# Kernel tuning notes

Hardware: AMD Instinct MI355X
Metric: run time of the kernel (lower is better)

## Reference

```python
import jax, jax.numpy as jnp
import numpy as np

D_MODEL = 768
NHEAD = 12
HEAD_DIM = D_MODEL // NHEAD
WINDOW = 33  # band half-width = 16


def setup_inputs() -> dict:
    key = jax.random.key(0)
    ks = jax.random.split(key, 9)
    B, T, C = 2, 4096, D_MODEL
    s = 0.02
    return {
        "x": jax.random.normal(ks[0], (B, T, C), jnp.float32),
        "Wq": jax.random.normal(ks[1], (C, C), jnp.float32) * s,
        "bq": jnp.zeros((C,), jnp.float32),
        "Wk": jax.random.normal(ks[2], (C, C), jnp.float32) * s,
        "bk": jnp.zeros((C,), jnp.float32),
        "Wv": jax.random.normal(ks[3], (C, C), jnp.float32) * s,
        "bv": jnp.zeros((C,), jnp.float32),
        "Wo": jax.random.normal(ks[4], (C, C), jnp.float32) * s,
        "bo": jnp.zeros((C,), jnp.float32),
    }


def reference(x, Wq, bq, Wk, bk, Wv, bv, Wo, bo):
    B, T, C = x.shape
    H, D = NHEAD, HEAD_DIM
    scale = D ** -0.5
    # torch Linear: x @ W.T + b
    q = (x @ Wq.T + bq).reshape(B, T, H, D).transpose(0, 2, 1, 3)  # [B,H,T,D]
    k = (x @ Wk.T + bk).reshape(B, T, H, D).transpose(0, 2, 1, 3)
    v = (x @ Wv.T + bv).reshape(B, T, H, D).transpose(0, 2, 1, 3)
    scores = jnp.einsum("bhqd,bhkd->bhqk", q, k) * scale  # [B,H,T,T]
    idx = jnp.arange(T)
    local_mask = jnp.abs(idx[:, None] - idx[None, :]) <= (WINDOW // 2)  # [T,T]
    scores = jnp.where(local_mask[None, None], scores, -jnp.inf)
    attn = jax.nn.softmax(scores, axis=-1)  # dropout=0 / eval mode
    out = jnp.einsum("bhqk,bhkd->bhqd", attn, v)  # [B,H,T,D]
    out = out.transpose(0, 2, 1, 3).reshape(B, T, C)
    return out @ Wo.T + bo
```

## Files before the change

### kernel.cpp

```cpp
#include <hip/hip_runtime.h>
#include <math.h>
#include <cstdint>
#include <cstddef>

typedef unsigned short u16;
typedef short bf16x8 __attribute__((ext_vector_type(8)));
typedef float f32x4 __attribute__((ext_vector_type(4)));
typedef u16 u16x8 __attribute__((ext_vector_type(8)));
typedef u16 u16x4 __attribute__((ext_vector_type(4)));

#define T_LEN 4096
#define NH 12
#define HD 64
#define DMODEL 768
#define GK 768
#define QKV_STRIDE 6291456ul

__device__ __forceinline__ u16 f2bf(float x) {
  union { float f; unsigned u; } v; v.f = x;
  unsigned r = v.u + 0x7fffu + ((v.u >> 16) & 1u);
  return (u16)(r >> 16);
}

__device__ __forceinline__ void async16(const u16* g, u16* l) {
  __builtin_amdgcn_global_load_lds(
      (const __attribute__((address_space(1))) unsigned int*)g,
      (__attribute__((address_space(3))) unsigned int*)l, 16, 0, 0);
}

__global__ void cvt_all(const float* __restrict__ x,
                        const float* __restrict__ Wq, const float* __restrict__ Wk,
                        const float* __restrict__ Wv, const float* __restrict__ Wo,
                        u16* __restrict__ xb, u16* __restrict__ wqkv, u16* __restrict__ wo_b) {
  int bx = blockIdx.x;
  const float* s; u16* d; int base;
  if (bx < 6144)      { s = x;  d = xb;             base = bx; }
  else if (bx < 6720) { s = Wq; d = wqkv;           base = bx - 6144; }
  else if (bx < 7296) { s = Wk; d = wqkv + 589824;  base = bx - 6720; }
  else if (bx < 7872) { s = Wv; d = wqkv + 1179648; base = bx - 7296; }
  else                { s = Wo; d = wo_b;           base = bx - 7872; }
  int i = (base * 256 + (int)threadIdx.x) * 4;
  float4 v = *(const float4*)(s + i);
  u16x4 o;
  o[0] = f2bf(v.x); o[1] = f2bf(v.y); o[2] = f2bf(v.z); o[3] = f2bf(v.w);
  *(u16x4*)(d + i) = o;
}

#define BN 128
#define BK 32
#define CPAD 8

template <int EPI, int MI, int NX, int NW>
__global__ __launch_bounds__(NW * 64)
void gemm_bt(const u16* __restrict__ A, const u16* __restrict__ B,
             const float* __restrict__ bias0, const float* __restrict__ bias1,
             const float* __restrict__ bias2, void* __restrict__ outp) {
  constexpr int NT   = NW * 64;
  constexpr int BMt  = (NW == 8) ? 256 : MI * 32;
  constexpr int NSTEP = GK / BK;
  constexpr int PER = NX / 8;
  constexpr int STG = 3 * (BMt + BN) * BK * 2;
  constexpr int CSZ = (EPI == 3) ? BMt * (BN + CPAD) * 2
                                 : 64 * 132 * 4;
  constexpr int SMEM = STG > CSZ ? STG : CSZ;
  __shared__ __align__(16) char smem[SMEM];
  u16* AsB = (u16*)smem;
  u16* BsB = (u16*)smem + 3 * BMt * BK;

  const int bid  = blockIdx.x;
  const int xcd  = bid & 7;
  const int slot = bid >> 3;
  const int bx   = xcd * PER + (slot % PER);
  const int by   = slot / PER;

  const int tid  = threadIdx.x;
  const int lane = tid & 63;
  const int wave = tid >> 6;
  const int wm = (NW == 8) ? (wave >> 1) : (wave & 1);
  const int wn = (NW == 8) ? (wave & 1)  : (wave >> 1);
  const long am0 = (long)bx * BMt;
  const long bn0 = (long)by * BN;
  const int r16 = lane & 15;
  const int kh  = lane >> 4;
  const int sw8 = (kh ^ ((r16 >> 1) & 3)) * 8;

  f32x4 acc[MI][4] = {};

  const int srow   = lane >> 2;
  const int schunk = ((lane & 3) ^ ((lane >> 3) & 3)) * 8;
  const u16* Ag = A + (am0 + wave * 16 + srow) * GK + schunk;
  const u16* Bg = B + (bn0 + wave * 16 + srow) * GK + schunk;

  auto stage = [&](int buf, int kt) {
    u16* Ab = AsB + buf * (BMt * BK);
    u16* Bb = BsB + buf * (BN * BK);
    if constexpr (NW == 8) {
#pragma unroll
      for (int s2 = 0; s2 < 2; s2++)
        async16(Ag + (size_t)(s2 * 128) * GK + kt, &Ab[(s2 * 128 + wave * 16) * BK]);
      async16(Bg + kt, &Bb[(wave * 16) * BK]);
    } else {
#pragma unroll
      for (int s2 = 0; s2 < MI / 2; s2++)
        async16(Ag + (size_t)(s2 * 64) * GK + kt, &Ab[(s2 * 64 + wave * 16) * BK]);
      async16(Bg + kt, &Bb[(wave * 16) * BK]);
      async16(Bg + (size_t)64 * GK + kt, &Bb[(64 + wave * 16) * BK]);
    }
  };

  stage(0, 0);
  stage(1, BK);
  int cur = 0;
  for (int s = 0; s < NSTEP; ++s) {
    if (s + 1 < NSTEP) {
      if constexpr (NW == 8)      asm volatile("s_waitcnt vmcnt(3)" ::: "memory");
      else if constexpr (MI == 4) asm volatile("s_waitcnt vmcnt(4)" ::: "memory");
      else                        asm volatile("s_waitcnt vmcnt(3)" ::: "memory");
    } else {
      asm volatile("s_waitcnt vmcnt(0)" ::: "memory");
    }
    __builtin_amdgcn_s_barrier();
    asm volatile("" ::: "memory");
    const u16* Ac = AsB + cur * (BMt * BK);
    const u16* Bc = BsB + cur * (BN * BK);
    bf16x8 af[MI], bfr[4];
#pragma unroll
    for (int i = 0; i < MI; i++)
      af[i] = *(const bf16x8*)&Ac[(wm * MI * 16 + i * 16 + r16) * BK + sw8];
#pragma unroll
    for (int j = 0; j < 4; j++)
      bfr[j] = *(const bf16x8*)&Bc[(wn * 64 + j * 16 + r16) * BK + sw8];
    if (s + 2 < NSTEP) {
      int c2 = cur + 2; if (c2 >= 3) c2 -= 3;
      stage(c2, (s + 2) * BK);
    }
#pragma unroll
    for (int i = 0; i < MI; i++)
#pragma unroll
      for (int j = 0; j < 4; j++)
        acc[i][j] = __builtin_amdgcn_mfma_f32_16x16x32_bf16(af[i], bfr[j], acc[i][j], 0, 0, 0);
    cur = (cur == 2) ? 0 : cur + 1;
  }
  __syncthreads();

  const int m0 = (int)am0 + wm * MI * 16;

  if (EPI == 3) {
    if (bn0 < 1536) {
      const int tens = (int)(bn0 >= 768);
      const int c0 = (int)bn0 - tens * 768;
      const float* bp = tens ? bias1 : bias0;
      u16* outb = (u16*)outp + (size_t)tens * QKV_STRIDE;
      u16* Cs = (u16*)smem;
#pragma unroll
      for (int j = 0; j < 4; j++) {
        int lc = wn * 64 + j * 16 + r16;
        float bv = bp[c0 + lc];
#pragma unroll
        for (int i = 0; i < MI; i++) {
          int lr = wm * MI * 16 + i * 16 + kh * 4;
#pragma unroll
          for (int r = 0; r < 4; r++)
            Cs[(lr + r) * (BN + CPAD) + lc] = f2bf(acc[i][j][r] + bv);
        }
      }
      __syncthreads();
#pragma unroll
      for (int z = 0; z < BMt * 16 / NT; z++) {
        int cidx = z * NT + tid;
        int row = cidx >> 4, ch = (cidx & 15) * 8;
        uint4 val = *(const uint4*)&Cs[row * (BN + CPAD) + ch];
        *(uint4*)(outb + (size_t)(am0 + row) * DMODEL + c0 + ch) = val;
      }
    } else {
      u16* vtb = (u16*)outp + 2 * QKV_STRIDE;
      const int kr = kh * 4;
#pragma unroll
      for (int j = 0; j < 4; j++) {
        int cl = (int)(bn0 - 1536) + wn * 64 + j * 16;
        int hj = cl >> 6;
        int dlane = (cl & 63) + r16;
        float bv = bias2[cl + r16];
#pragma unroll
        for (int i = 0; i < MI; i++) {
          int row0 = m0 + i * 16;
          int b_ = row0 >> 12;
          int tb = (row0 & 4095) >> 4;
          size_t base = (((size_t)(b_ * NH + hj) * 256 + tb) << 10) + dlane * 16 + kr;
          u16x4 pk;
#pragma unroll
          for (int r = 0; r < 4; r++) pk[r] = f2bf(acc[i][j][r] + bv);
          *(u16x4*)(vtb + base) = pk;
        }
      }
    }
  } else {
    float* Cf = (float*)smem;
#pragma unroll
    for (int j = 0; j < 4; j++) {
      int lc = wn * 64 + j * 16 + r16;
      float bv = bias0[(int)bn0 + lc];
#pragma unroll
      for (int i = 0; i < MI; i++) {
        int lr = wm * MI * 16 + i * 16 + kh * 4;
#pragma unroll
        for (int r = 0; r < 4; r++)
          Cf[(lr + r) * 132 + lc] = acc[i][j][r] + bv;
      }
    }
    __syncthreads();
    float* O = (float*)outp;
#pragma unroll
    for (int z = 0; z < 8; z++) {
      int idx = z * 256 + tid;
      int row = idx >> 5, c4 = (idx & 31) * 4;
      float4 v = *(const float4*)&Cf[row * 132 + c4];
      *(float4*)(O + (size_t)(am0 + row) * DMODEL + bn0 + c4) = v;
    }
  }
}

#define PSS 72

__global__ __launch_bounds__(256)
void attn_mfma(const u16* __restrict__ qkv, const u16* __restrict__ vt,
               u16* __restrict__ attn) {
  __shared__ __align__(16) u16 Ps[4][16 * PSS];
  const int tid = threadIdx.x, lane = tid & 63, wave = tid >> 6;
  const int r16 = lane & 15, quad = lane >> 4;
  const int q0 = blockIdx.x * 64;
  const int h = blockIdx.y, b = blockIdx.z;
  const long rowbase = (long)b * T_LEN;
  const int hc = h * HD;
  const u16* Qg = qkv;
  const u16* Kg = qkv + QKV_STRIDE;
  const u16* Vh = vt + ((size_t)(b * NH + h)) * (256 * 1024);

  const int qbase = q0 + wave * 16;
  const int kb = qbase - 16;

  const u16* qrow = Qg + (rowbase + qbase + r16) * DMODEL + hc + quad * 8;
  bf16x8 qa0 = *(const bf16x8*)qrow;
  bf16x8 qa1 = *(const bf16x8*)(qrow + 32);

  f32x4 s[3];
#pragma unroll
  for (int t = 0; t < 3; t++) {
    const u16* krow = Kg + (rowbase + kb + t * 16 + r16) * DMODEL + hc + quad * 8;
    bf16x8 kf0 = *(const bf16x8*)krow;
    bf16x8 kf1 = *(const bf16x8*)(krow + 32);
    f32x4 a = {};
    __builtin_amdgcn_s_setprio(1);
    a = __builtin_amdgcn_mfma_f32_16x16x32_bf16(qa0, kf0, a, 0, 0, 0);
    a = __builtin_amdgcn_mfma_f32_16x16x32_bf16(qa1, kf1, a, 0, 0, 0);
    __builtin_amdgcn_s_setprio(0);
    s[t] = a;
  }

  float pr[3][4];
#pragma unroll
  for (int r = 0; r < 4; r++) {
    const int qg = qbase + quad * 4 + r;
    float sc[3];
#pragma unroll
    for (int t = 0; t < 3; t++) {
      int key = kb + t * 16 + r16;
      bool ok = (key >= qg - 16) && (key <= qg + 16) && (key >= 0) && (key < T_LEN);
      sc[t] = ok ? s[t][r] * 0.125f : -INFINITY;
    }
    float mx = fmaxf(sc[0], fmaxf(sc[1], sc[2]));
    mx = fmaxf(mx, __shfl_xor(mx, 1));
    mx = fmaxf(mx, __shfl_xor(mx, 2));
    mx = fmaxf(mx, __shfl_xor(mx, 4));
    mx = fmaxf(mx, __shfl_xor(mx, 8));
    float e0 = __expf(sc[0] - mx), e1 = __expf(sc[1] - mx), e2 = __expf(sc[2] - mx);
    float l = e0 + e1 + e2;
    l += __shfl_xor(l, 1);
    l += __shfl_xor(l, 2);
    l += __shfl_xor(l, 4);
    l += __shfl_xor(l, 8);
    float inv = 1.0f / l;
    pr[0][r] = e0 * inv; pr[1][r] = e1 * inv; pr[2][r] = e2 * inv;
  }

  u16* psw = &Ps[wave][0];
#pragma unroll
  for (int t = 0; t < 3; t++)
#pragma unroll
    for (int r = 0; r < 4; r++)
      psw[(quad * 4 + r) * PSS + t * 16 + r16] = f2bf(pr[t][r]);
#pragma unroll
  for (int r = 0; r < 4; r++)
    psw[(quad * 4 + r) * PSS + 48 + r16] = 0;

  bf16x8 pa0 = *(const bf16x8*)&psw[r16 * PSS + quad * 8];
  bf16x8 pa1 = *(const bf16x8*)&psw[r16 * PSS + 32 + quad * 8];

  const int kq1 = kb + quad * 8;
  const int kq2 = kb + 32 + quad * 8;
  const int o1 = (kq1 >> 4) * 1024 + (kq1 & 15);
  const int o2 = (kq2 >> 4) * 1024 + (kq2 & 15);
  f32x4 o[4];
#pragma unroll
  for (int c = 0; c < 4; c++) {
    const u16* vb = Vh + (16 * c + r16) * 16;
    bf16x8 v1 = *(const bf16x8*)(vb + o1);
    bf16x8 v2 = *(const bf16x8*)(vb + o2);
    f32x4 a = {};
    __builtin_amdgcn_s_setprio(1);
    a = __builtin_amdgcn_mfma_f32_16x16x32_bf16(pa0, v1, a, 0, 0, 0);
    a = __builtin_amdgcn_mfma_f32_16x16x32_bf16(pa1, v2, a, 0, 0, 0);
    __builtin_amdgcn_s_setprio(0);
    o[c] = a;
  }

#pragma unroll
  for (int c = 0; c < 4; c++)
#pragma unroll
    for (int r = 0; r < 4; r++)
      psw[(quad * 4 + r) * PSS + 16 * c + r16] = f2bf(o[c][r]);
  {
    int rr = lane >> 3, cc = (lane & 7) * 8;
    u16x8 v0 = *(const u16x8*)&psw[rr * PSS + cc];
    u16x8 v1 = *(const u16x8*)&psw[(8 + rr) * PSS + cc];
    u16* ob = attn + (rowbase + qbase) * DMODEL + hc;
    *(u16x8*)(ob + (size_t)rr * DMODEL + cc) = v0;
    *(u16x8*)(ob + (size_t)(8 + rr) * DMODEL + cc) = v1;
  }
}

extern "C" void kernel_launch(void* const* d_in, const int* in_sizes, int n_in,
                              void* d_out, int out_size, void* d_ws, size_t ws_size,
                              hipStream_t stream) {
  const float* x  = (const float*)d_in[0];
  const float* Wq = (const float*)d_in[1];
  const float* bq = (const float*)d_in[2];
  const float* Wk = (const float*)d_in[3];
  const float* bk = (const float*)d_in[4];
  const float* Wv = (const float*)d_in[5];
  const float* bv = (const float*)d_in[6];
  const float* Wo = (const float*)d_in[7];
  const float* bo = (const float*)d_in[8];
  float* out = (float*)d_out;
  char* ws = (char*)d_ws;

  u16* xb   = (u16*)(ws);
  u16* wqkv = (u16*)(ws + 12582912);
  u16* wo_b = (u16*)(ws + 16121856);
  u16* qkv  = (u16*)(ws + 17301504);
  u16* attnb = (u16*)(ws + 55050240);

  cvt_all<<<8448, 256, 0, stream>>>(x, Wq, Wk, Wv, Wo, xb, wqkv, wo_b);

  gemm_bt<3, 4, 32, 8><<<576, 512, 0, stream>>>(xb, wqkv, bq, bk, bv, (void*)qkv);
  attn_mfma<<<dim3(64, 12, 2), 256, 0, stream>>>(qkv, qkv + 2 * QKV_STRIDE, attnb);
  gemm_bt<1, 2, 128, 4><<<768, 256, 0, stream>>>(attnb, wo_b, bo, bo, bo, (void*)out);
}
```

Baseline: 164.0 us.

## Shrink GEMM LDS footprint: double-buffer 8-wave tiles and split epilogue staging

For the 8-wave (256-row) GEMM configuration, the async staging pipeline drops from triple to double buffering, and the QKV epilogue staging buffer is halved by writing the C tile to LDS in two 128-row passes. This cuts LDS use per block, likely so more blocks fit per CU. In exchange the load pipeline has less prefetch depth, with a full vmcnt(0) wait each step, and the epilogue gains extra barriers. It also assumes EPI==3 only ever runs with 8 waves (BMt=256).

```diff
diff --git a/kernel.cpp b/kernel.cpp
--- a/kernel.cpp
+++ b/kernel.cpp
@@ -55,17 +55,18 @@
 void gemm_bt(const u16* __restrict__ A, const u16* __restrict__ B,
              const float* __restrict__ bias0, const float* __restrict__ bias1,
              const float* __restrict__ bias2, void* __restrict__ outp) {
-  constexpr int NT   = NW * 64;
-  constexpr int BMt  = (NW == 8) ? 256 : MI * 32;
+  constexpr int NT    = NW * 64;
+  constexpr int BMt   = (NW == 8) ? 256 : MI * 32;
+  constexpr int DEPTH = (NW == 8) ? 2 : 3;
   constexpr int NSTEP = GK / BK;
   constexpr int PER = NX / 8;
-  constexpr int STG = 3 * (BMt + BN) * BK * 2;
-  constexpr int CSZ = (EPI == 3) ? BMt * (BN + CPAD) * 2
+  constexpr int STG = DEPTH * (BMt + BN) * BK * 2;
+  constexpr int CSZ = (EPI == 3) ? (BMt / 2) * (BN + CPAD) * 2
                                  : 64 * 132 * 4;
   constexpr int SMEM = STG > CSZ ? STG : CSZ;
   __shared__ __align__(16) char smem[SMEM];
   u16* AsB = (u16*)smem;
-  u16* BsB = (u16*)smem + 3 * BMt * BK;
+  u16* BsB = (u16*)smem + DEPTH * BMt * BK;
 
   const int bid  = blockIdx.x;
   const int xcd  = bid & 7;
@@ -109,15 +110,18 @@
   };
 
   stage(0, 0);
-  stage(1, BK);
+  if constexpr (DEPTH == 3) stage(1, BK);
   int cur = 0;
   for (int s = 0; s < NSTEP; ++s) {
-    if (s + 1 < NSTEP) {
-      if constexpr (NW == 8)      asm volatile("s_waitcnt vmcnt(3)" ::: "memory");
-      else if constexpr (MI == 4) asm volatile("s_waitcnt vmcnt(4)" ::: "memory");
-      else                        asm volatile("s_waitcnt vmcnt(3)" ::: "memory");
+    if constexpr (DEPTH == 2) {
+      asm volatile("s_waitcnt vmcnt(0)" ::: "memory");
     } else {
-      asm volatile("s_waitcnt vmcnt(0)" ::: "memory");
+      if (s + 1 < NSTEP) {
+        if constexpr (MI == 4) asm volatile("s_waitcnt vmcnt(4)" ::: "memory");
+        else                   asm volatile("s_waitcnt vmcnt(3)" ::: "memory");
+      } else {
+        asm volatile("s_waitcnt vmcnt(0)" ::: "memory");
+      }
     }
     __builtin_amdgcn_s_barrier();
     asm volatile("" ::: "memory");
@@ -130,22 +134,22 @@
 #pragma unroll
     for (int j = 0; j < 4; j++)
       bfr[j] = *(const bf16x8*)&Bc[(wn * 64 + j * 16 + r16) * BK + sw8];
-    if (s + 2 < NSTEP) {
-      int c2 = cur + 2; if (c2 >= 3) c2 -= 3;
-      stage(c2, (s + 2) * BK);
+    if (s + DEPTH - 1 < NSTEP) {
+      int c2 = cur + DEPTH - 1; if (c2 >= DEPTH) c2 -= DEPTH;
+      stage(c2, (s + DEPTH - 1) * BK);
     }
 #pragma unroll
     for (int i = 0; i < MI; i++)
 #pragma unroll
       for (int j = 0; j < 4; j++)
         acc[i][j] = __builtin_amdgcn_mfma_f32_16x16x32_bf16(af[i], bfr[j], acc[i][j], 0, 0, 0);
-    cur = (cur == 2) ? 0 : cur + 1;
+    cur = cur + 1; if (cur >= DEPTH) cur = 0;
   }
   __syncthreads();
 
   const int m0 = (int)am0 + wm * MI * 16;
 
-  if (EPI == 3) {
+  if constexpr (EPI == 3) {
     if (bn0 < 1536) {
       const int tens = (int)(bn0 >= 768);
       const int c0 = (int)bn0 - tens * 768;
@@ -153,24 +157,30 @@
       u16* outb = (u16*)outp + (size_t)tens * QKV_STRIDE;
       u16* Cs = (u16*)smem;
 #pragma unroll
-      for (int j = 0; j < 4; j++) {
-        int lc = wn * 64 + j * 16 + r16;
-        float bv = bp[c0 + lc];
-#pragma unroll
-        for (int i = 0; i < MI; i++) {
-          int lr = wm * MI * 16 + i * 16 + kh * 4;
-#pragma unroll
-          for (int r = 0; r < 4; r++)
-            Cs[(lr + r) * (BN + CPAD) + lc] = f2bf(acc[i][j][r] + bv);
+      for (int p = 0; p < 2; p++) {
+        if ((wm >> 1) == p) {
+#pragma unroll
+          for (int j = 0; j < 4; j++) {
+            int lc = wn * 64 + j * 16 + r16;
+            float bv = bp[c0 + lc];
+#pragma unroll
+            for (int i = 0; i < MI; i++) {
+              int lr = (wm & 1) * 64 + i * 16 + kh * 4;
+#pragma unroll
+              for (int r = 0; r < 4; r++)
+                Cs[(lr + r) * (BN + CPAD) + lc] = f2bf(acc[i][j][r] + bv);
+            }
+          }
         }
-      }
-      __syncthreads();
-#pragma unroll
-      for (int z = 0; z < BMt * 16 / NT; z++) {
-        int cidx = z * NT + tid;
-        int row = cidx >> 4, ch = (cidx & 15) * 8;
-        uint4 val = *(const uint4*)&Cs[row * (BN + CPAD) + ch];
-        *(uint4*)(outb + (size_t)(am0 + row) * DMODEL + c0 + ch) = val;
+        __syncthreads();
+#pragma unroll
+        for (int z = 0; z < 2048 / NT; z++) {
+          int cidx = z * NT + tid;
+          int row = cidx >> 4, ch = (cidx & 15) * 8;
+          uint4 val = *(const uint4*)&Cs[row * (BN + CPAD) + ch];
+          *(uint4*)(outb + (size_t)(am0 + p * 128 + row) * DMODEL + c0 + ch) = val;
+        }
+        __syncthreads();
       }
     } else {
       u16* vtb = (u16*)outp + 2 * QKV_STRIDE;
```

Measured after the change: 170.2 us. 3.8% more time.
